# Kernel tuning notes

Hardware: AMD Instinct MI355X
Metric: run time of the kernel (lower is better)

## Reference

```python
import jax, jax.numpy as jnp
import numpy as np


def setup_inputs() -> dict:
    key = jax.random.key(0)
    ks = jax.random.split(key, 8)
    B, T, U = 4, 256, 128
    E, D, J, V = 512, 640, 640, 1024
    enc = jax.random.normal(ks[0], (B, T, E), dtype=jnp.float32)
    dec = jax.random.normal(ks[1], (B, U, D), dtype=jnp.float32)
    # Linear params (kaiming-uniform-ish scale is irrelevant for correctness; use scaled normals)
    W_enc = jax.random.normal(ks[2], (E, J), dtype=jnp.float32) / np.sqrt(E)
    b_enc = jax.random.normal(ks[3], (J,), dtype=jnp.float32) * 0.01
    W_dec = jax.random.normal(ks[4], (D, J), dtype=jnp.float32) / np.sqrt(D)
    b_dec = jax.random.normal(ks[5], (J,), dtype=jnp.float32) * 0.01
    W_joint = jax.random.normal(ks[6], (J, V), dtype=jnp.float32) / np.sqrt(J)
    b_joint = jax.random.normal(ks[7], (V,), dtype=jnp.float32) * 0.01
    return {
        "encoder_outputs": enc,
        "decoder_outputs": dec,
        "W_enc": W_enc, "b_enc": b_enc,
        "W_dec": W_dec, "b_dec": b_dec,
        "W_joint": W_joint, "b_joint": b_joint,
    }


def reference(encoder_outputs, decoder_outputs, W_enc, b_enc, W_dec, b_dec, W_joint, b_joint):
    # enc_proj: (B,T,J); dec_proj: (B,U,J)
    enc_proj = jnp.einsum('bte,ej->btj', encoder_outputs, W_enc) + b_enc
    dec_proj = jnp.einsum('bud,dj->buj', decoder_outputs, W_dec) + b_dec
    # broadcast add -> (B,T,U,J), tanh, then project to vocab
    joint = jnp.tanh(enc_proj[:, :, None, :] + dec_proj[:, None, :, :])
    logits = jnp.einsum('btuj,jv->btuv', joint, W_joint) + b_joint
    return logits
```

## Files before the change

kernel.cpp:

```cpp
#include <hip/hip_runtime.h>
#include <stdint.h>

typedef float  f4     __attribute__((ext_vector_type(4)));
typedef float  f32x4  __attribute__((ext_vector_type(4)));
typedef __bf16 bf16x8 __attribute__((ext_vector_type(8)));

#define AS_GLOBAL __attribute__((address_space(1)))
#define AS_LDS    __attribute__((address_space(3)))

constexpr int Bdim = 4, T = 256, U = 128, E = 512, Dd = 640, J = 640, V = 1024;
constexpr int BM = 128, BN = 128, BK = 32;

__device__ __forceinline__ void lds_load16(void* lds, const void* g) {
  __builtin_amdgcn_global_load_lds(
      (const AS_GLOBAL uint32_t*)(uintptr_t)g,
      (AS_LDS uint32_t*)(uint32_t)(uintptr_t)lds, 16, 0, 0);
}

__device__ __forceinline__ float fast_tanh(float x) {
  float e = __builtin_amdgcn_exp2f(x * 2.88539008177f);
  return 1.0f - 2.0f * __builtin_amdgcn_rcpf(e + 1.0f);
}

__global__ __launch_bounds__(256) void proj_kernel(
    const float* __restrict__ X, const float* __restrict__ W,
    const float* __restrict__ bias, float* __restrict__ out, int K) {
  const int tid = threadIdx.x;
  const int jt  = tid & 127;
  const int h   = tid >> 7;
  const int r0  = blockIdx.x * 4;
  __shared__ float sX[4 * 640];
  __shared__ float sAcc[4 * 5 * 128];

  for (int idx = tid * 4; idx < 4 * K; idx += 1024)
    *(f4*)&sX[idx] = *(const f4*)&X[(size_t)r0 * K + idx];
  __syncthreads();

  float acc[4][5] = {};
  const int e0 = h * (K >> 1), e1 = e0 + (K >> 1);
  for (int e = e0; e < e1; e += 4) {
    f4 xr[4];
#pragma unroll
    for (int r = 0; r < 4; ++r) xr[r] = *(const f4*)&sX[r * K + e];
#pragma unroll
    for (int i = 0; i < 4; ++i) {
#pragma unroll
      for (int q = 0; q < 5; ++q) {
        float w = W[(size_t)(e + i) * J + q * 128 + jt];
#pragma unroll
        for (int r = 0; r < 4; ++r) acc[r][q] = fmaf(xr[r][i], w, acc[r][q]);
      }
    }
  }
  if (h == 1) {
#pragma unroll
    for (int r = 0; r < 4; ++r)
#pragma unroll
      for (int q = 0; q < 5; ++q) sAcc[(r * 5 + q) * 128 + jt] = acc[r][q];
  }
  __syncthreads();
  if (h == 0) {
#pragma unroll
    for (int r = 0; r < 4; ++r)
#pragma unroll
      for (int q = 0; q < 5; ++q) {
        float v = acc[r][q] + sAcc[(r * 5 + q) * 128 + jt] + bias[q * 128 + jt];
        out[(size_t)(r0 + r) * J + q * 128 + jt] = v;
      }
  }
}

__global__ __launch_bounds__(256) void transpose_wj(const float* __restrict__ W,
                                                    __bf16* __restrict__ Wt) {
  __shared__ float t[32][33];
  const int v0 = blockIdx.x * 32, j0 = blockIdx.y * 32;
  const int c = threadIdx.x & 31, r = threadIdx.x >> 5;
#pragma unroll
  for (int rr = 0; rr < 4; ++rr)
    t[r + rr * 8][c] = W[(size_t)(j0 + r + rr * 8) * V + v0 + c];
  __syncthreads();
#pragma unroll
  for (int rr = 0; rr < 4; ++rr)
    Wt[(size_t)(v0 + r + rr * 8) * J + j0 + c] = (__bf16)t[c][r + rr * 8];
}

__global__ __launch_bounds__(256) void joint_kernel(
    const float* __restrict__ ep, const float* __restrict__ dp,
    const __bf16* __restrict__ Wt, const float* __restrict__ bj,
    float* __restrict__ out) {
  const int bt  = blockIdx.y;
  const int v0  = blockIdx.x * BN;
  const int b   = bt >> 8;
  const int tid = threadIdx.x;
  const int wave = tid >> 6, lane = tid & 63;

  __shared__ __align__(16) __bf16 As[BM * BK];
  __shared__ __align__(16) __bf16 Bs[BN * BK];

  const float* epr = ep + (size_t)bt * J;
  const float* dpr = dp + (size_t)b * U * J;

  const int su = tid >> 2;
  const int sk = (tid & 3) * 8;

  const int wm = (wave >> 1) * 64, wn = (wave & 1) * 64;
  const int lrow = lane & 15, lq = lane >> 4;

  f32x4 acc[4][4] = {};

  for (int k0 = 0; k0 < J; k0 += BK) {
#pragma unroll
    for (int p = 0; p < 2; ++p) {
      const __bf16* src = Wt + (size_t)(v0 + p * 64 + su) * J + k0 + sk;
      lds_load16(Bs + p * 2048 + tid * 8, src);
    }
#pragma unroll
    for (int p = 0; p < 2; ++p) {
      const int u = p * 64 + su;
      const float* dsrc = dpr + (size_t)u * J + k0 + sk;
      f4 d0 = *(const f4*)dsrc;
      f4 d1 = *(const f4*)(dsrc + 4);
      f4 e0 = *(const f4*)(epr + k0 + sk);
      f4 e1 = *(const f4*)(epr + k0 + sk + 4);
      bf16x8 av;
#pragma unroll
      for (int i = 0; i < 4; ++i) av[i]     = (__bf16)fast_tanh(d0[i] + e0[i]);
#pragma unroll
      for (int i = 0; i < 4; ++i) av[i + 4] = (__bf16)fast_tanh(d1[i] + e1[i]);
      *(bf16x8*)(As + u * BK + sk) = av;
    }
    __syncthreads();
    bf16x8 af[4], bf[4];
#pragma unroll
    for (int f = 0; f < 4; ++f) {
      af[f] = *(const bf16x8*)(As + (wm + f * 16 + lrow) * BK + lq * 8);
      bf[f] = *(const bf16x8*)(Bs + (wn + f * 16 + lrow) * BK + lq * 8);
    }
#pragma unroll
    for (int fm = 0; fm < 4; ++fm)
#pragma unroll
      for (int fn = 0; fn < 4; ++fn)
        acc[fm][fn] = __builtin_amdgcn_mfma_f32_16x16x32_bf16(af[fm], bf[fn], acc[fm][fn], 0, 0, 0);
    __syncthreads();
  }

  const size_t rowbase = (size_t)bt * U;
#pragma unroll
  for (int fn = 0; fn < 4; ++fn) {
    const int col = v0 + wn + fn * 16 + lrow;
    const float bv = bj[col];
#pragma unroll
    for (int fm = 0; fm < 4; ++fm) {
      const int u = wm + fm * 16 + lq * 4;
#pragma unroll
      for (int i = 0; i < 4; ++i)
        out[(rowbase + u + i) * (size_t)V + col] = acc[fm][fn][i] + bv;
    }
  }
}

extern "C" void kernel_launch(void* const* d_in, const int* in_sizes, int n_in,
                              void* d_out, int out_size, void* d_ws, size_t ws_size,
                              hipStream_t stream) {
  (void)in_sizes; (void)n_in; (void)out_size; (void)ws_size;
  const float* enc    = (const float*)d_in[0];
  const float* dec    = (const float*)d_in[1];
  const float* W_enc  = (const float*)d_in[2];
  const float* b_enc  = (const float*)d_in[3];
  const float* W_dec  = (const float*)d_in[4];
  const float* b_dec  = (const float*)d_in[5];
  const float* W_jnt  = (const float*)d_in[6];
  const float* b_jnt  = (const float*)d_in[7];
  float* out = (float*)d_out;

  float*  ep = (float*)d_ws;
  float*  dp = ep + (size_t)Bdim * T * J;
  __bf16* Wt = (__bf16*)(dp + (size_t)Bdim * U * J);

  proj_kernel<<<dim3(Bdim * T / 4), 256, 0, stream>>>(enc, W_enc, b_enc, ep, E);
  proj_kernel<<<dim3(Bdim * U / 4), 256, 0, stream>>>(dec, W_dec, b_dec, dp, Dd);
  transpose_wj<<<dim3(V / 32, J / 32), 256, 0, stream>>>(W_jnt, Wt);
  joint_kernel<<<dim3(V / BN, Bdim * T), 256, 0, stream>>>(ep, dp, Wt, b_jnt, out);
}
```

Baseline: 1.024 ms.

## Retile joint GEMM to 64x256x64 with XOR-swizzled LDS and bias-initialized accumulators

Changes the joint kernel tile from 128x128x32 to 64 rows by 256 vocab columns with K-step 64. Both LDS tiles get an XOR swizzle to avoid bank conflicts, and the bias is folded into the accumulator init. Launch bounds now request 3 blocks per CU. Each tanh row is computed once per 256 vocab columns instead of per 128, which halves redundant tanh work, but each block now reads more of Wt per K-step and holds a larger LDS footprint.

```diff
diff --git a/kernel.cpp b/kernel.cpp
--- a/kernel.cpp
+++ b/kernel.cpp
@@ -9,7 +9,6 @@
 #define AS_LDS    __attribute__((address_space(3)))
 
 constexpr int Bdim = 4, T = 256, U = 128, E = 512, Dd = 640, J = 640, V = 1024;
-constexpr int BM = 128, BN = 128, BK = 32;
 
 __device__ __forceinline__ void lds_load16(void* lds, const void* g) {
   __builtin_amdgcn_global_load_lds(
@@ -84,77 +83,96 @@
     Wt[(size_t)(v0 + r + rr * 8) * J + j0 + c] = (__bf16)t[c][r + rr * 8];
 }
 
-__global__ __launch_bounds__(256) void joint_kernel(
+constexpr int JBM = 64, JBN = 256, JBK = 64;
+
+__global__ __launch_bounds__(256, 3) void joint_kernel(
     const float* __restrict__ ep, const float* __restrict__ dp,
     const __bf16* __restrict__ Wt, const float* __restrict__ bj,
     float* __restrict__ out) {
-  const int bt  = blockIdx.y;
-  const int v0  = blockIdx.x * BN;
-  const int b   = bt >> 8;
-  const int tid = threadIdx.x;
-  const int wave = tid >> 6, lane = tid & 63;
-
-  __shared__ __align__(16) __bf16 As[BM * BK];
-  __shared__ __align__(16) __bf16 Bs[BN * BK];
+  const int mblk = blockIdx.y;
+  const int bt   = mblk >> 1;
+  const int u0   = (mblk & 1) * JBM;
+  const int b    = bt >> 8;
+  const int v0   = blockIdx.x * JBN;
+  const int tid  = threadIdx.x;
+  const int wv   = tid >> 6, lane = tid & 63;
+  const int lrow = lane & 15, lq = lane >> 4;
+
+  __shared__ __align__(16) __bf16 As[JBM * JBK];
+  __shared__ __align__(16) __bf16 Bs[JBN * JBK];
 
   const float* epr = ep + (size_t)bt * J;
-  const float* dpr = dp + (size_t)b * U * J;
-
-  const int su = tid >> 2;
-  const int sk = (tid & 3) * 8;
-
-  const int wm = (wave >> 1) * 64, wn = (wave & 1) * 64;
-  const int lrow = lane & 15, lq = lane >> 4;
-
-  f32x4 acc[4][4] = {};
-
-  for (int k0 = 0; k0 < J; k0 += BK) {
-#pragma unroll
-    for (int p = 0; p < 2; ++p) {
-      const __bf16* src = Wt + (size_t)(v0 + p * 64 + su) * J + k0 + sk;
-      lds_load16(Bs + p * 2048 + tid * 8, src);
-    }
-#pragma unroll
-    for (int p = 0; p < 2; ++p) {
-      const int u = p * 64 + su;
-      const float* dsrc = dpr + (size_t)u * J + k0 + sk;
-      f4 d0 = *(const f4*)dsrc;
-      f4 d1 = *(const f4*)(dsrc + 4);
-      f4 e0 = *(const f4*)(epr + k0 + sk);
-      f4 e1 = *(const f4*)(epr + k0 + sk + 4);
+  const float* dpr = dp + ((size_t)b * U + u0) * J;
+
+  f32x4 acc[4][4];
+#pragma unroll
+  for (int fn = 0; fn < 4; ++fn) {
+    const float bv = bj[v0 + wv * 64 + fn * 16 + lrow];
+#pragma unroll
+    for (int fm = 0; fm < 4; ++fm) acc[fm][fn] = (f32x4){bv, bv, bv, bv};
+  }
+
+  const int ar = tid >> 3;
+  const int as = tid & 7;
+  const int aw = (as ^ (ar & 7));
+
+  for (int k0 = 0; k0 < J; k0 += JBK) {
+    {
+      const int ssrc = as ^ (ar & 7);
+      const __bf16* src0 = Wt + (size_t)(v0 + ar) * J + k0 + ssrc * 8;
+#pragma unroll
+      for (int i = 0; i < 8; ++i)
+        lds_load16((char*)Bs + (size_t)(i * 256 + tid) * 16,
+                   src0 + (size_t)i * 32 * J);
+    }
+#pragma unroll
+    for (int hh = 0; hh < 2; ++hh) {
+      const int r = ar + hh * 32;
+      const float* ds = dpr + (size_t)r * J + k0 + as * 8;
+      const float* es = epr + k0 + as * 8;
+      f4 d0 = *(const f4*)ds, d1 = *(const f4*)(ds + 4);
+      f4 e0 = *(const f4*)es, e1 = *(const f4*)(es + 4);
       bf16x8 av;
 #pragma unroll
       for (int i = 0; i < 4; ++i) av[i]     = (__bf16)fast_tanh(d0[i] + e0[i]);
 #pragma unroll
       for (int i = 0; i < 4; ++i) av[i + 4] = (__bf16)fast_tanh(d1[i] + e1[i]);
-      *(bf16x8*)(As + u * BK + sk) = av;
+      *(bf16x8*)((char*)As + r * 128 + aw * 16) = av;
     }
     __syncthreads();
-    bf16x8 af[4], bf[4];
-#pragma unroll
-    for (int f = 0; f < 4; ++f) {
-      af[f] = *(const bf16x8*)(As + (wm + f * 16 + lrow) * BK + lq * 8);
-      bf[f] = *(const bf16x8*)(Bs + (wn + f * 16 + lrow) * BK + lq * 8);
-    }
-#pragma unroll
-    for (int fm = 0; fm < 4; ++fm)
-#pragma unroll
-      for (int fn = 0; fn < 4; ++fn)
-        acc[fm][fn] = __builtin_amdgcn_mfma_f32_16x16x32_bf16(af[fm], bf[fn], acc[fm][fn], 0, 0, 0);
+
+#pragma unroll
+    for (int hh = 0; hh < 2; ++hh) {
+      bf16x8 af[4], bfr[4];
+#pragma unroll
+      for (int f = 0; f < 4; ++f) {
+        const int rm = f * 16 + lrow;
+        af[f] = *(const bf16x8*)((char*)As + rm * 128 +
+                                 (((lq + 4 * hh) ^ (rm & 7)) * 16));
+        const int rn = wv * 64 + f * 16 + lrow;
+        bfr[f] = *(const bf16x8*)((char*)Bs + rn * 128 +
+                                  (((lq + 4 * hh) ^ (rn & 7)) * 16));
+      }
+#pragma unroll
+      for (int fm = 0; fm < 4; ++fm)
+#pragma unroll
+        for (int fn = 0; fn < 4; ++fn)
+          acc[fm][fn] = __builtin_amdgcn_mfma_f32_16x16x32_bf16(
+              af[fm], bfr[fn], acc[fm][fn], 0, 0, 0);
+    }
     __syncthreads();
   }
 
-  const size_t rowbase = (size_t)bt * U;
+  const size_t rowbase = (size_t)bt * U + u0;
 #pragma unroll
   for (int fn = 0; fn < 4; ++fn) {
-    const int col = v0 + wn + fn * 16 + lrow;
-    const float bv = bj[col];
+    const int col = v0 + wv * 64 + fn * 16 + lrow;
 #pragma unroll
     for (int fm = 0; fm < 4; ++fm) {
-      const int u = wm + fm * 16 + lq * 4;
+      const int u = fm * 16 + lq * 4;
 #pragma unroll
       for (int i = 0; i < 4; ++i)
-        out[(rowbase + u + i) * (size_t)V + col] = acc[fm][fn][i] + bv;
+        out[(rowbase + u + i) * (size_t)V + col] = acc[fm][fn][i];
     }
   }
 }
@@ -180,5 +198,5 @@
   proj_kernel<<<dim3(Bdim * T / 4), 256, 0, stream>>>(enc, W_enc, b_enc, ep, E);
   proj_kernel<<<dim3(Bdim * U / 4), 256, 0, stream>>>(dec, W_dec, b_dec, dp, Dd);
   transpose_wj<<<dim3(V / 32, J / 32), 256, 0, stream>>>(W_jnt, Wt);
-  joint_kernel<<<dim3(V / BN, Bdim * T), 256, 0, stream>>>(ep, dp, Wt, b_jnt, out);
-}
+  joint_kernel<<<dim3(V / JBN, Bdim * T * U / JBM), 256, 0, stream>>>(ep, dp, Wt, b_jnt, out);
+}
```

Measured after the change: 851.8 us. 1.2x faster.
